# Performance work log

Hardware: AMD Instinct MI355X
Metric: run time of the kernel (lower is better)

## Reference

```python
import jax, jax.numpy as jnp
import numpy as np

NUM_EMBEDDINGS = 1024  # num_gestures
EMBEDDING_DIM = 512    # win_size * num_pellets = 32 * 16


def setup_inputs() -> dict:
    key = jax.random.key(0)
    k1, k2 = jax.random.split(key)
    inputs = jax.random.normal(k1, (64, 512, EMBEDDING_DIM), dtype=jnp.float32)
    weight = jax.random.normal(k2, (NUM_EMBEDDINGS, EMBEDDING_DIM), dtype=jnp.float32)
    return {"inputs": inputs, "weight": weight}


def reference(inputs, weight):
    input_shape = inputs.shape
    flat = inputs.reshape(-1, EMBEDDING_DIM)  # [N, D]
    distances = (
        jnp.sum(flat * flat, axis=1, keepdims=True)
        + jnp.sum(weight * weight, axis=1)
        - 2.0 * (flat @ weight.T)
    )
    encoding_indices = jnp.argmin(distances, axis=1)  # [N]
    # one-hot @ weight is just a gather of codebook rows
    quantized = weight[encoding_indices].reshape(input_shape)
    loss_vq = jnp.mean((quantized - inputs) ** 2)
    return loss_vq
```

## Files before the change

### kernel.cpp

```cpp
#include <hip/hip_runtime.h>
#include <hip/hip_bf16.h>
#include <stdint.h>

typedef __attribute__((ext_vector_type(4))) int i32x4;

#define N_ROWS  32768
#define N_CODES 1024
#define DIM     512

typedef const __attribute__((address_space(1))) uint32_t guint;
typedef __attribute__((address_space(3))) uint32_t luint;
static __device__ __forceinline__ void gl_lds16(const char* g, char* l) {
    __builtin_amdgcn_global_load_lds((guint*)g, (luint*)l, 16, 0, 0);
}

static __device__ __forceinline__ int q8(float v) {
    int q = __float2int_rn(v * 32.0f);
    return max(-127, min(127, q));
}
static __device__ __forceinline__ uint32_t pack4(float a, float b, float c, float d) {
    return (uint32_t)(q8(a) & 0xFF) | ((uint32_t)(q8(b) & 0xFF) << 8)
         | ((uint32_t)(q8(c) & 0xFF) << 16) | ((uint32_t)(q8(d) & 0xFF) << 24);
}

__global__ void __launch_bounds__(256)
convertW(const float* __restrict__ W, char* __restrict__ Wq,
         float* __restrict__ wnorm) {
    const int lane = threadIdx.x & 63;
    const int code = blockIdx.x * 4 + (threadIdx.x >> 6);
    const float4* p = (const float4*)(W + (size_t)code * DIM + lane * 8);
    float4 a = p[0], b = p[1];
    *(uint2*)(Wq + (size_t)code * DIM + lane * 8) =
        make_uint2(pack4(a.x, a.y, a.z, a.w), pack4(b.x, b.y, b.z, b.w));
    float s = a.x*a.x + a.y*a.y + a.z*a.z + a.w*a.w
            + b.x*b.x + b.y*b.y + b.z*b.z + b.w*b.w;
    #pragma unroll
    for (int d = 1; d < 64; d <<= 1) s += __shfl_xor(s, d);
    if (lane == 0) wnorm[code] = s;
}

__global__ void __launch_bounds__(256, 2)
gemm_argmin(const float* __restrict__ X, const char* __restrict__ Wq,
            const float* __restrict__ wnorm, float* __restrict__ partial) {
    __shared__ __align__(16) char As[8 * 4096];
    __shared__ __align__(16) char Bs[4 * 3 * 4096];

    const int tid  = threadIdx.x;
    const int lane = tid & 63;
    const int wave = tid >> 6;
    const int lr = lane & 15, kg = lane >> 4;

    const int bid = blockIdx.x;
    const int rowBase = ((bid & 7) * 64 + (bid >> 3)) * 64;
    const int colW = wave * 256;

    const int ssw = ((lane & 3) ^ ((lane >> 3) & 3)) * 16;
    const char* bS = Wq + (size_t)(colW + (lane >> 2)) * DIM + ssw;
    char* bD = Bs + wave * 12288 + lane * 16;

#define STAGE_B(s) do {                                                       \
    const int ctp_ = (s) >> 3, kt_ = (s) & 7, buf_ = (s) % 3;                 \
    _Pragma("unroll")                                                         \
    for (int j = 0; j < 4; ++j)                                               \
        gl_lds16(bS + (size_t)(ctp_ * 64 + j * 16) * DIM + kt_ * 64,          \
                 bD + buf_ * 4096 + j * 1024);                                \
  } while (0)

    STAGE_B(0);
    STAGE_B(1);

    const int r = tid >> 2, q4 = tid & 3;
    const int rsw = (r >> 1) & 3;
    float nrm = 0.f;
    {
        const float* xP = X + (size_t)(rowBase + r) * DIM + q4 * 128;
        #pragma unroll
        for (int c = 0; c < 8; ++c) {
            float4 f0 = *(const float4*)(xP + c * 16);
            float4 f1 = *(const float4*)(xP + c * 16 + 4);
            float4 f2 = *(const float4*)(xP + c * 16 + 8);
            float4 f3 = *(const float4*)(xP + c * 16 + 12);
            nrm += f0.x*f0.x + f0.y*f0.y + f0.z*f0.z + f0.w*f0.w
                 + f1.x*f1.x + f1.y*f1.y + f1.z*f1.z + f1.w*f1.w
                 + f2.x*f2.x + f2.y*f2.y + f2.z*f2.z + f2.w*f2.w
                 + f3.x*f3.x + f3.y*f3.y + f3.z*f3.z + f3.w*f3.w;
            i32x4 v = { (int)pack4(f0.x, f0.y, f0.z, f0.w),
                        (int)pack4(f1.x, f1.y, f1.z, f1.w),
                        (int)pack4(f2.x, f2.y, f2.z, f2.w),
                        (int)pack4(f3.x, f3.y, f3.z, f3.w) };
            const int kt = 2 * q4 + (c >> 2), sl = c & 3;
            *(i32x4*)&As[kt * 4096 + r * 64 + (sl ^ rsw) * 16] = v;
        }
        nrm += __shfl_xor(nrm, 1);
        nrm += __shfl_xor(nrm, 2);
    }
    __syncthreads();

    i32x4 acc[4][4];
    #pragma unroll
    for (int m = 0; m < 4; ++m)
        #pragma unroll
        for (int n = 0; n < 4; ++n) acc[m][n] = (i32x4)0;
    uint32_t runKey[4][4];
    #pragma unroll
    for (int m = 0; m < 4; ++m)
        #pragma unroll
        for (int rr = 0; rr < 4; ++rr) runKey[m][rr] = 0xFFFFFFFFu;

    const int fq = (kg ^ ((lr >> 1) & 3)) * 16;
    const char* bR = Bs + wave * 12288;

    for (int ctp = 0; ctp < 4; ++ctp) {
        #pragma unroll
        for (int kt = 0; kt < 8; ++kt) {
            const int s = ctp * 8 + kt;
            const int buf = s % 3;
            i32x4 aF[4], bF[4];
            #pragma unroll
            for (int m = 0; m < 4; ++m)
                aF[m] = *(const i32x4*)&As[kt * 4096 + (m * 16 + lr) * 64 + fq];
            #pragma unroll
            for (int n = 0; n < 4; ++n)
                bF[n] = *(const i32x4*)&bR[buf * 4096 + (n * 16 + lr) * 64 + fq];
            if (s + 2 < 32) STAGE_B(s + 2);
            #pragma unroll
            for (int m = 0; m < 4; ++m)
                #pragma unroll
                for (int n = 0; n < 4; ++n)
                    acc[m][n] = __builtin_amdgcn_mfma_i32_16x16x64_i8(
                        aF[m], bF[n], acc[m][n], 0, 0, 0);
            if (s + 2 < 32)   asm volatile("s_waitcnt vmcnt(4)" ::: "memory");
            else if (s == 30) asm volatile("s_waitcnt vmcnt(0)" ::: "memory");
        }
        #pragma unroll
        for (int n = 0; n < 4; ++n) {
            const int wcol = colW + ctp * 64 + n * 16 + lr;
            const float wn = wnorm[wcol];
            #pragma unroll
            for (int m = 0; m < 4; ++m)
                #pragma unroll
                for (int rr = 0; rr < 4; ++rr) {
                    float sc = wn - (float)acc[m][n][rr] * 0.001953125f;
                    uint32_t u = __float_as_uint(sc);
                    u = (u & 0x80000000u) ? ~u : (u | 0x80000000u);
                    runKey[m][rr] = min(runKey[m][rr],
                                        (u & ~1023u) | (uint32_t)wcol);
                }
        }
        #pragma unroll
        for (int m = 0; m < 4; ++m)
            #pragma unroll
            for (int n = 0; n < 4; ++n) acc[m][n] = (i32x4)0;
    }
#undef STAGE_B

    uint32_t* kbuf = (uint32_t*)(Bs + wave * 12288);
    #pragma unroll
    for (int m = 0; m < 4; ++m)
        #pragma unroll
        for (int rr = 0; rr < 4; ++rr) {
            uint32_t k = runKey[m][rr];
            #pragma unroll
            for (int d = 1; d < 16; d <<= 1)
                k = min(k, (uint32_t)__shfl_xor((int)k, d));
            if (lr == 0) kbuf[m * 16 + kg * 4 + rr] = k;
        }
    float* xnS = (float*)(Bs + 48896);
    if ((tid & 3) == 0) xnS[r] = nrm;
    __syncthreads();

    if (wave == 0) {
        const uint32_t* k0 = (const uint32_t*)(Bs);
        uint32_t k = min(min(k0[lane], k0[3072 + lane]),
                         min(k0[6144 + lane], k0[9216 + lane]));
        uint32_t sb = k & ~1023u;
        float sc = (sb & 0x80000000u) ? __uint_as_float(sb ^ 0x80000000u)
                                      : __uint_as_float(~sb);
        float v = xnS[lane] + sc;
        #pragma unroll
        for (int d = 1; d < 64; d <<= 1) v += __shfl_xor(v, d);
        if (lane == 0) partial[bid] = v;
    }
}

__global__ void __launch_bounds__(256)
finalize(const float* __restrict__ partial, float* __restrict__ out) {
    __shared__ double sm[256];
    sm[threadIdx.x] = (double)partial[threadIdx.x]
                    + (double)partial[threadIdx.x + 256];
    __syncthreads();
    for (int st = 128; st > 0; st >>= 1) {
        if (threadIdx.x < st) sm[threadIdx.x] += sm[threadIdx.x + st];
        __syncthreads();
    }
    if (threadIdx.x == 0)
        out[0] = (float)(sm[0] / (double)((size_t)N_ROWS * DIM));
}

extern "C" void kernel_launch(void* const* d_in, const int* in_sizes, int n_in,
                              void* d_out, int out_size, void* d_ws, size_t ws_size,
                              hipStream_t stream) {
    const float* X = (const float*)d_in[0];
    const float* W = (const float*)d_in[1];
    char* ws = (char*)d_ws;
    char*   Wq      = ws;
    float*  wnorm   = (float*)(ws + 524288);
    float*  partial = (float*)(ws + 528384);
    float*  out     = (float*)d_out;

    convertW<<<N_CODES / 4, 256, 0, stream>>>(W, Wq, wnorm);
    gemm_argmin<<<512, 256, 0, stream>>>(X, Wq, wnorm, partial);
    finalize<<<1, 256, 0, stream>>>(partial, out);
}
```

Measured before the change: 47.47 us.

## Switch int8 argmin GEMM to 32x32x32 MFMA with halved B staging

Replaces the 16x16x64 int8 MFMA tiling with 32x32x32 MFMA (2x2 accumulators of 16 ints each), which changes fragment layouts, LDS swizzles and the K-step count (64 steps of 32 instead of 32 of 64). B staging buffers shrink to 2 KB per stage and the codebook norms are preloaded into registers rather than read inside the loop. Intended to cut LDS fragment-read traffic per MFMA and raise MFMA efficiency. In exchange there are more pipeline iterations and waitcnts, and the cross-lane argmin reduction becomes 32-wide.

After: 59.86 us. 26.1% more time.

```diff
diff --git a/kernel.cpp b/kernel.cpp
--- a/kernel.cpp
+++ b/kernel.cpp
@@ -2,7 +2,8 @@
 #include <hip/hip_bf16.h>
 #include <stdint.h>
 
-typedef __attribute__((ext_vector_type(4))) int i32x4;
+typedef __attribute__((ext_vector_type(4)))  int i32x4;
+typedef __attribute__((ext_vector_type(16))) int i32x16;
 
 #define N_ROWS  32768
 #define N_CODES 1024
@@ -43,27 +44,30 @@
 gemm_argmin(const float* __restrict__ X, const char* __restrict__ Wq,
             const float* __restrict__ wnorm, float* __restrict__ partial) {
     __shared__ __align__(16) char As[8 * 4096];
-    __shared__ __align__(16) char Bs[4 * 3 * 4096];
+    __shared__ __align__(16) char Bs[4 * 3 * 2048];
+    __shared__ float xnS[64];
 
     const int tid  = threadIdx.x;
     const int lane = tid & 63;
     const int wave = tid >> 6;
-    const int lr = lane & 15, kg = lane >> 4;
+    const int l31 = lane & 31, kh = lane >> 5;
+    const int arsw = (l31 >> 1) & 3;
+    const int brsw = (l31 >> 2) & 1;
 
     const int bid = blockIdx.x;
     const int rowBase = ((bid & 7) * 64 + (bid >> 3)) * 64;
     const int colW = wave * 256;
 
-    const int ssw = ((lane & 3) ^ ((lane >> 3) & 3)) * 16;
-    const char* bS = Wq + (size_t)(colW + (lane >> 2)) * DIM + ssw;
-    char* bD = Bs + wave * 12288 + lane * 16;
+    const char* bS = Wq + (size_t)(colW + (lane >> 1)) * DIM
+                   + (((lane & 1) ^ ((lane >> 3) & 1)) * 16);
+    char* bD = Bs + wave * 6144 + lane * 16;
 
 #define STAGE_B(s) do {                                                       \
-    const int ctp_ = (s) >> 3, kt_ = (s) & 7, buf_ = (s) % 3;                 \
+    const int ctp_ = (s) >> 4, kt_ = (s) & 15, buf_ = (s) % 3;                \
     _Pragma("unroll")                                                         \
-    for (int j = 0; j < 4; ++j)                                               \
-        gl_lds16(bS + (size_t)(ctp_ * 64 + j * 16) * DIM + kt_ * 64,          \
-                 bD + buf_ * 4096 + j * 1024);                                \
+    for (int j = 0; j < 2; ++j)                                               \
+        gl_lds16(bS + (size_t)(ctp_ * 64 + j * 32) * DIM + kt_ * 32,          \
+                 bD + buf_ * 2048 + j * 1024);                                \
   } while (0)
 
     STAGE_B(0);
@@ -93,86 +97,94 @@
         }
         nrm += __shfl_xor(nrm, 1);
         nrm += __shfl_xor(nrm, 2);
-    }
+        if ((tid & 3) == 0) xnS[r] = nrm;
+    }
+    float wnR[4][2];
+    #pragma unroll
+    for (int c = 0; c < 4; ++c)
+        #pragma unroll
+        for (int n = 0; n < 2; ++n)
+            wnR[c][n] = wnorm[colW + c * 64 + n * 32 + l31];
     __syncthreads();
 
-    i32x4 acc[4][4];
-    #pragma unroll
-    for (int m = 0; m < 4; ++m)
-        #pragma unroll
-        for (int n = 0; n < 4; ++n) acc[m][n] = (i32x4)0;
-    uint32_t runKey[4][4];
-    #pragma unroll
-    for (int m = 0; m < 4; ++m)
-        #pragma unroll
-        for (int rr = 0; rr < 4; ++rr) runKey[m][rr] = 0xFFFFFFFFu;
-
-    const int fq = (kg ^ ((lr >> 1) & 3)) * 16;
-    const char* bR = Bs + wave * 12288;
+    i32x16 acc[2][2];
+    #pragma unroll
+    for (int m = 0; m < 2; ++m)
+        #pragma unroll
+        for (int n = 0; n < 2; ++n) acc[m][n] = (i32x16)0;
+    uint32_t runKey[2][16];
+    #pragma unroll
+    for (int m = 0; m < 2; ++m)
+        #pragma unroll
+        for (int g = 0; g < 16; ++g) runKey[m][g] = 0xFFFFFFFFu;
+
+    const char* bR = Bs + wave * 6144;
 
     for (int ctp = 0; ctp < 4; ++ctp) {
         #pragma unroll
-        for (int kt = 0; kt < 8; ++kt) {
-            const int s = ctp * 8 + kt;
+        for (int kt = 0; kt < 16; ++kt) {
+            const int s = ctp * 16 + kt;
             const int buf = s % 3;
-            i32x4 aF[4], bF[4];
-            #pragma unroll
-            for (int m = 0; m < 4; ++m)
-                aF[m] = *(const i32x4*)&As[kt * 4096 + (m * 16 + lr) * 64 + fq];
-            #pragma unroll
-            for (int n = 0; n < 4; ++n)
-                bF[n] = *(const i32x4*)&bR[buf * 4096 + (n * 16 + lr) * 64 + fq];
-            if (s + 2 < 32) STAGE_B(s + 2);
-            #pragma unroll
-            for (int m = 0; m < 4; ++m)
+            i32x4 aF[2], bF[2];
+            #pragma unroll
+            for (int m = 0; m < 2; ++m)
+                aF[m] = *(const i32x4*)&As[(kt >> 1) * 4096
+                        + (m * 32 + l31) * 64
+                        + ((((kt & 1) * 2 + kh) ^ arsw) * 16)];
+            #pragma unroll
+            for (int n = 0; n < 2; ++n)
+                bF[n] = *(const i32x4*)&bR[buf * 2048
+                        + (n * 32 + l31) * 32 + ((kh ^ brsw) * 16)];
+            if (s + 2 < 64) STAGE_B(s + 2);
+            #pragma unroll
+            for (int m = 0; m < 2; ++m)
                 #pragma unroll
-                for (int n = 0; n < 4; ++n)
-                    acc[m][n] = __builtin_amdgcn_mfma_i32_16x16x64_i8(
+                for (int n = 0; n < 2; ++n)
+                    acc[m][n] = __builtin_amdgcn_mfma_i32_32x32x32_i8(
                         aF[m], bF[n], acc[m][n], 0, 0, 0);
-            if (s + 2 < 32)   asm volatile("s_waitcnt vmcnt(4)" ::: "memory");
-            else if (s == 30) asm volatile("s_waitcnt vmcnt(0)" ::: "memory");
-        }
-        #pragma unroll
-        for (int n = 0; n < 4; ++n) {
-            const int wcol = colW + ctp * 64 + n * 16 + lr;
-            const float wn = wnorm[wcol];
-            #pragma unroll
-            for (int m = 0; m < 4; ++m)
+            if (s + 2 < 64)   asm volatile("s_waitcnt vmcnt(2)" ::: "memory");
+            else if (s == 62) asm volatile("s_waitcnt vmcnt(0)" ::: "memory");
+        }
+        #pragma unroll
+        for (int n = 0; n < 2; ++n) {
+            const int wcol = colW + ctp * 64 + n * 32 + l31;
+            const float wn = wnR[ctp][n];
+            #pragma unroll
+            for (int m = 0; m < 2; ++m)
                 #pragma unroll
-                for (int rr = 0; rr < 4; ++rr) {
-                    float sc = wn - (float)acc[m][n][rr] * 0.001953125f;
+                for (int g = 0; g < 16; ++g) {
+                    float sc = wn - (float)acc[m][n][g] * 0.001953125f;
                     uint32_t u = __float_as_uint(sc);
                     u = (u & 0x80000000u) ? ~u : (u | 0x80000000u);
-                    runKey[m][rr] = min(runKey[m][rr],
-                                        (u & ~1023u) | (uint32_t)wcol);
+                    runKey[m][g] = min(runKey[m][g],
+                                       (u & ~1023u) | (uint32_t)wcol);
                 }
         }
         #pragma unroll
-        for (int m = 0; m < 4; ++m)
-            #pragma unroll
-            for (int n = 0; n < 4; ++n) acc[m][n] = (i32x4)0;
+        for (int m = 0; m < 2; ++m)
+            #pragma unroll
+            for (int n = 0; n < 2; ++n) acc[m][n] = (i32x16)0;
     }
 #undef STAGE_B
 
-    uint32_t* kbuf = (uint32_t*)(Bs + wave * 12288);
-    #pragma unroll
-    for (int m = 0; m < 4; ++m)
-        #pragma unroll
-        for (int rr = 0; rr < 4; ++rr) {
-            uint32_t k = runKey[m][rr];
-            #pragma unroll
-            for (int d = 1; d < 16; d <<= 1)
+    uint32_t* kbuf = (uint32_t*)(Bs + wave * 6144);
+    #pragma unroll
+    for (int m = 0; m < 2; ++m)
+        #pragma unroll
+        for (int g = 0; g < 16; ++g) {
+            uint32_t k = runKey[m][g];
+            #pragma unroll
+            for (int d = 1; d < 32; d <<= 1)
                 k = min(k, (uint32_t)__shfl_xor((int)k, d));
-            if (lr == 0) kbuf[m * 16 + kg * 4 + rr] = k;
-        }
-    float* xnS = (float*)(Bs + 48896);
-    if ((tid & 3) == 0) xnS[r] = nrm;
+            if (l31 == 0)
+                kbuf[m * 32 + (g & 3) + 8 * (g >> 2) + 4 * kh] = k;
+        }
     __syncthreads();
 
     if (wave == 0) {
         const uint32_t* k0 = (const uint32_t*)(Bs);
-        uint32_t k = min(min(k0[lane], k0[3072 + lane]),
-                         min(k0[6144 + lane], k0[9216 + lane]));
+        uint32_t k = min(min(k0[lane], k0[1536 + lane]),
+                         min(k0[3072 + lane], k0[4608 + lane]));
         uint32_t sb = k & ~1023u;
         float sc = (sb & 0x80000000u) ? __uint_as_float(sb ^ 0x80000000u)
                                       : __uint_as_float(~sb);
```
